# Optimization experiments

Measured on AMD Instinct MI355X. Metric: run time of the kernel, lower is better.

Reference implementation:

```python
import jax, jax.numpy as jnp
import numpy as np

B, L, D, H, M = 4, 2048, 256, 8, 256
HEAD = D // H
EPS = 1e-6


def _pos_embedding(maxlen, d):
    i = np.arange(maxlen, dtype=np.float64)[:, None]
    j = np.arange(d, dtype=np.float64)[None, :]
    angle = i / np.power(10000.0, (j - (j % 2)) / d)
    pe = np.where(j % 2 == 0, np.sin(angle), np.cos(angle))
    return jnp.asarray(pe, jnp.float32)  # [L, D]


def _projection_matrix(m, d, seed=0):
    # FAVOR+ orthogonal random features: one full QR block (m == d here),
    # rows rescaled by norms of iid Gaussian rows (scaling=0 in source).
    rng = np.random.default_rng(seed)
    block = rng.standard_normal((d, d))
    q, _ = np.linalg.qr(block)
    q = q.T[:m]
    mult = np.linalg.norm(rng.standard_normal((m, d)), axis=1)
    return jnp.asarray(mult[:, None] * q, jnp.float32)  # [M, D]


def _softmax_kernel(x, is_query, proj):
    # x: [B, L, H, D], proj: [M, D]
    d = x.shape[-1]
    m = proj.shape[0]
    x = x * (float(d) ** -0.25)
    xp = jnp.einsum('blhd,md->blhm', x, proj)
    diag = 0.5 * jnp.sum(x * x, axis=-1, keepdims=True)
    if is_query:
        mx = jnp.max(xp, axis=-1, keepdims=True)
    else:
        mx = jnp.max(xp, axis=(-3, -1), keepdims=True)  # over L and M
    return (float(m) ** -0.5) * (jnp.exp(xp - diag - mx) + EPS)


def setup_inputs() -> dict:
    key = jax.random.key(0)
    ks = jax.random.split(key, 12)
    s = 1.0 / np.sqrt(D)
    inp = {
        'query': jax.random.normal(ks[0], (B, L, D), jnp.float32),
        'key': jax.random.normal(ks[1], (B, L, D), jnp.float32),
        'value': jax.random.normal(ks[2], (B, L, D), jnp.float32),
        'mask': jnp.ones((B, L), jnp.float32),
        'Wq': jax.random.normal(ks[3], (D, D), jnp.float32) * s,
        'bq': jnp.zeros((D,), jnp.float32),
        'Wk': jax.random.normal(ks[4], (D, D), jnp.float32) * s,
        'bk': jnp.zeros((D,), jnp.float32),
        'Wv': jax.random.normal(ks[5], (D, D), jnp.float32) * s,
        'bv': jnp.zeros((D,), jnp.float32),
        'Wo': jax.random.normal(ks[6], (D, D), jnp.float32) * s,
        'bo': jnp.zeros((D,), jnp.float32),
        'proj': _projection_matrix(M, D, seed=0),
        'pos': _pos_embedding(L, D),
    }
    return inp


def reference(query, key, value, mask, Wq, bq, Wk, bk, Wv, bv, Wo, bo, proj, pos):
    b = query.shape[0]
    q = query @ Wq + bq                      # [B, L, D]
    k = key @ Wk + bk
    v = value @ Wv + bv
    # per-head copies keep the FULL model_size feature dim (as in source)
    q = jnp.broadcast_to(q[:, :, None, :], (b, L, H, D))
    k = jnp.broadcast_to(k[:, :, None, :], (b, L, H, D))
    pos_b = pos[None]                        # [1, L, D]
    cos_pos = jnp.repeat(pos_b[..., None, 1::2], 2, axis=-1)  # [1, L, 1, D]
    sin_pos = jnp.repeat(pos_b[..., None, ::2], 2, axis=-1)

    def rot(x):
        x2 = jnp.stack([-x[..., 1::2], x[..., ::2]], axis=-1).reshape(x.shape)
        return x * cos_pos + x2 * sin_pos

    q = rot(q)
    k = rot(k)
    v = v.reshape(b, L, H, HEAD)

    qp = _softmax_kernel(q, True, proj)      # [B, L, H, M]
    kp = _softmax_kernel(k, False, proj)     # [B, L, H, M]

    kvs = jnp.einsum('blhm,blhd->bhmd', kp, v)
    num = jnp.einsum('blhm,bhmd->blhd', qp, kvs)
    den = jnp.einsum('blhm,bhm->blh', qp, jnp.sum(kp, axis=1))
    ctx = (num / den[..., None]).reshape(b, L, D)
    return ctx @ Wo + bo
```

## Files before the change

### kernel.cpp

```cpp
#include <hip/hip_runtime.h>

typedef unsigned short u16;
typedef unsigned int u32;
typedef __bf16 bf16x8 __attribute__((ext_vector_type(8)));
typedef float f32x4 __attribute__((ext_vector_type(4)));

__device__ __forceinline__ float bf2f(u16 u) { return __uint_as_float(((u32)u) << 16); }
__device__ __forceinline__ u16 f2bf(float f) {
  u32 x = __float_as_uint(f);
  x += 0x7fffu + ((x >> 16) & 1u);
  return (u16)(x >> 16);
}
__device__ __forceinline__ u32 encf(float x) {
  u32 u = __float_as_uint(x);
  return (u >> 31) ? ~u : (u | 0x80000000u);
}
__device__ __forceinline__ float decf(u32 e) {
  return (e >> 31) ? __uint_as_float(e & 0x7fffffffu) : __uint_as_float(~e);
}

#define MFMA(a, b, c) __builtin_amdgcn_mfma_f32_16x16x32_bf16(a, b, c, 0, 0, 0)

__global__ __launch_bounds__(256) void prep_w(
    const float* Wq, const float* Wk, const float* Wv, const float* Wo,
    const float* proj, const float* bv,
    u16* WqT, u16* WkT, u16* projb, u16* WWT, float* bw,
    float* __restrict__ ksum, u32* __restrict__ mxk) {
  __shared__ u16 tsh[32][33];
  __shared__ u16 As[64][40];
  __shared__ u16 Bs[64][40];
  const int z = blockIdx.z;
  const int x = threadIdx.x, y = threadIdx.y;
  const int tid = y * 32 + x;
  if (z < 2) {
    const float* s = z == 0 ? Wq : Wk;
    u16* d = z == 0 ? WqT : WkT;
    int r0 = blockIdx.y * 32, c0 = blockIdx.x * 32;
#pragma unroll
    for (int i = 0; i < 32; i += 8) tsh[y + i][x] = f2bf(s[(r0 + y + i) * 256 + c0 + x]);
    __syncthreads();
#pragma unroll
    for (int i = 0; i < 32; i += 8) d[(c0 + y + i) * 256 + r0 + x] = tsh[x][y + i];
    return;
  }
  if (z == 2) {
    int r0 = blockIdx.y * 32, c0 = blockIdx.x * 32;
#pragma unroll
    for (int i = 0; i < 32; i += 8)
      projb[(r0 + y + i) * 256 + c0 + x] = f2bf(proj[(r0 + y + i) * 256 + c0 + x]);
    return;
  }
  if (blockIdx.x < 4 && blockIdx.y < 4) {
    const int o0 = blockIdx.x * 64, i0 = blockIdx.y * 64;
    const int lane = tid & 63, wid = tid >> 6;
    const int wm = (wid >> 1) * 32, wn = (wid & 1) * 32;
    const int fm = lane & 15, fq = (lane >> 4) * 8, rowq = (lane >> 4) * 4;
    const int dr = tid >> 3, oc = (tid & 7) * 8;
    const int ir = tid >> 2, dc = (tid & 3) * 8;
    f32x4 acc[2][2] = {};
    for (int it = 0; it < 8; ++it) {
      int d0 = it * 32;
      float4 w0 = *(const float4*)(Wo + (d0 + dr) * 256 + o0 + oc);
      float4 w1 = *(const float4*)(Wo + (d0 + dr) * 256 + o0 + oc + 4);
      float4 v0 = *(const float4*)(Wv + (i0 + ir) * 256 + d0 + dc);
      float4 v1 = *(const float4*)(Wv + (i0 + ir) * 256 + d0 + dc + 4);
      __syncthreads();
      float wv[8] = {w0.x, w0.y, w0.z, w0.w, w1.x, w1.y, w1.z, w1.w};
#pragma unroll
      for (int j = 0; j < 8; ++j) As[oc + j][dr] = f2bf(wv[j]);
      u16* bp = &Bs[ir][dc];
      bp[0] = f2bf(v0.x); bp[1] = f2bf(v0.y); bp[2] = f2bf(v0.z); bp[3] = f2bf(v0.w);
      bp[4] = f2bf(v1.x); bp[5] = f2bf(v1.y); bp[6] = f2bf(v1.z); bp[7] = f2bf(v1.w);
      __syncthreads();
      bf16x8 a0 = *(const bf16x8*)&As[wm + fm][fq];
      bf16x8 a1 = *(const bf16x8*)&As[wm + 16 + fm][fq];
      bf16x8 b0 = *(const bf16x8*)&Bs[wn + fm][fq];
      bf16x8 b1 = *(const bf16x8*)&Bs[wn + 16 + fm][fq];
      acc[0][0] = MFMA(a0, b0, acc[0][0]);
      acc[0][1] = MFMA(a0, b1, acc[0][1]);
      acc[1][0] = MFMA(a1, b0, acc[1][0]);
      acc[1][1] = MFMA(a1, b1, acc[1][1]);
    }
#pragma unroll
    for (int mt = 0; mt < 2; ++mt)
#pragma unroll
      for (int nt = 0; nt < 2; ++nt)
#pragma unroll
        for (int r = 0; r < 4; ++r)
          WWT[(o0 + wm + mt * 16 + rowq + r) * 256 + i0 + wn + nt * 16 + fm] =
              f2bf(acc[mt][nt][r]);
    return;
  }
  if (blockIdx.x == 4 && blockIdx.y == 0) {
    float s = 0.0f;
    for (int d = 0; d < 256; ++d) s = fmaf(bv[d], Wo[d * 256 + tid], s);
    bw[tid] = s;
    for (int i = tid; i < 1024; i += 256) ksum[i] = 0.0f;
    if (tid < 4) mxk[tid] = 0u;
  }
}

__global__ __launch_bounds__(256, 3) void projrot2(
    const float* __restrict__ Xq, const float* __restrict__ Xk,
    const u16* __restrict__ WqT, const u16* __restrict__ WkT,
    const float* __restrict__ bq, const float* __restrict__ bk,
    const float* __restrict__ pos, const u16* __restrict__ projb,
    float* __restrict__ diag_k, u16* __restrict__ qp,
    float* __restrict__ xp, u32* __restrict__ mxk) {
  const int mode = blockIdx.z;
  const float* X = mode ? Xq : Xk;
  const u16* W = mode ? WqT : WkT;
  const float* bias = mode ? bq : bk;
  __shared__ u16 As[32][40];
  __shared__ u16 Bs[256][40];
  __shared__ u16 cbuf[32][264];
  __shared__ float dred[2][32];
  __shared__ float mred[2][32];
  __shared__ float wred[4];
  const int row0 = blockIdx.x * 32;
  const int t = threadIdx.x;
  const int lane = t & 63, wid = t >> 6;
  const int wrow = wid & 1, wcol = wid >> 1;
  const int fm = lane & 15, fq = (lane >> 4) * 8, rowq = (lane >> 4) * 4;
  const int ar = t >> 3, ak = (t & 7) * 4;

  f32x4 acc[8] = {};
  float4 av = *(const float4*)(X + (long long)(row0 + ar) * 256 + ak);
  uint4 bv0 = ((const uint4*)(W + (long long)t * 256))[0];
  uint4 bv1 = ((const uint4*)(W + (long long)t * 256))[1];
  uint4 bv2 = ((const uint4*)(W + (long long)t * 256))[2];
  uint4 bv3 = ((const uint4*)(W + (long long)t * 256))[3];
  for (int s = 0; s < 8; ++s) {
    __syncthreads();
    As[ar][ak] = f2bf(av.x); As[ar][ak + 1] = f2bf(av.y);
    As[ar][ak + 2] = f2bf(av.z); As[ar][ak + 3] = f2bf(av.w);
    uint4* bsp = (uint4*)&Bs[t][0];
    bsp[0] = bv0; bsp[1] = bv1; bsp[2] = bv2; bsp[3] = bv3;
    __syncthreads();
    if (s < 7) {
      const int k1 = (s + 1) * 32;
      av = *(const float4*)(X + (long long)(row0 + ar) * 256 + k1 + ak);
      const uint4* wn = (const uint4*)(W + (long long)t * 256 + k1);
      bv0 = wn[0]; bv1 = wn[1]; bv2 = wn[2]; bv3 = wn[3];
    }
    bf16x8 af = *(const bf16x8*)&As[wrow * 16 + fm][fq];
#pragma unroll
    for (int j = 0; j < 8; ++j) {
      bf16x8 bf = *(const bf16x8*)&Bs[wcol * 128 + j * 16 + fm][fq];
      acc[j] = MFMA(af, bf, acc[j]);
    }
  }

  float dsum[4] = {};
#pragma unroll
  for (int j = 0; j < 8; ++j) {
    float bb2 = bias[wcol * 128 + j * 16 + fm];
#pragma unroll
    for (int r = 0; r < 4; ++r) {
      float v = acc[j][r] + bb2;
      acc[j][r] = v;
      dsum[r] += v * v;
    }
  }
#pragma unroll
  for (int o = 1; o < 16; o <<= 1)
#pragma unroll
    for (int r = 0; r < 4; ++r) dsum[r] += __shfl_xor(dsum[r], o, 64);
  if (fm == 0) {
#pragma unroll
    for (int r = 0; r < 4; ++r) dred[wcol][wrow * 16 + rowq + r] = dsum[r];
  }
  __syncthreads();
  if (mode == 0 && t < 32) diag_k[row0 + t] = 0.03125f * (dred[0][t] + dred[1][t]);

#pragma unroll
  for (int j = 0; j < 8; ++j) {
    const int c = wcol * 128 + j * 16 + fm;
#pragma unroll
    for (int r = 0; r < 4; ++r) {
      const int row = wrow * 16 + rowq + r;
      const int l = (row0 + row) & 2047;
      float v = acc[j][r];
      float prt = __shfl_xor(v, 1, 64);
      float x2 = (fm & 1) ? prt : -prt;
      float2 cs = *(const float2*)(pos + (long long)l * 256 + (c & ~1));
      cbuf[row][c] = f2bf(0.25f * (v * cs.y + x2 * cs.x));
    }
  }

  f32x4 acc2[8] = {};
  uint4 pv0 = ((const uint4*)(projb + (long long)t * 256))[0];
  uint4 pv1 = ((const uint4*)(projb + (long long)t * 256))[1];
  uint4 pv2 = ((const uint4*)(projb + (long long)t * 256))[2];
  uint4 pv3 = ((const uint4*)(projb + (long long)t * 256))[3];
  for (int s = 0; s < 8; ++s) {
    __syncthreads();
    uint4* bsp = (uint4*)&Bs[t][0];
    bsp[0] = pv0; bsp[1] = pv1; bsp[2] = pv2; bsp[3] = pv3;
    __syncthreads();
    if (s < 7) {
      const uint4* pn = (const uint4*)(projb + (long long)t * 256 + (s + 1) * 32);
      pv0 = pn[0]; pv1 = pn[1]; pv2 = pn[2]; pv3 = pn[3];
    }
    bf16x8 af = *(const bf16x8*)&cbuf[wrow * 16 + fm][s * 32 + fq];
#pragma unroll
    for (int j = 0; j < 8; ++j) {
      bf16x8 bf = *(const bf16x8*)&Bs[wcol * 128 + j * 16 + fm][fq];
      acc2[j] = MFMA(af, bf, acc2[j]);
    }
  }

  if (mode == 1) {
    float m4[4] = {-3.0e38f, -3.0e38f, -3.0e38f, -3.0e38f};
#pragma unroll
    for (int j = 0; j < 8; ++j)
#pragma unroll
      for (int r = 0; r < 4; ++r) m4[r] = fmaxf(m4[r], acc2[j][r]);
#pragma unroll
    for (int o = 1; o < 16; o <<= 1)
#pragma unroll
      for (int r = 0; r < 4; ++r) m4[r] = fmaxf(m4[r], __shfl_xor(m4[r], o, 64));
    if (fm == 0) {
#pragma unroll
      for (int r = 0; r < 4; ++r) mred[wcol][wrow * 16 + rowq + r] = m4[r];
    }
    __syncthreads();
#pragma unroll
    for (int j = 0; j < 8; ++j) {
      const int col = wcol * 128 + j * 16 + fm;
#pragma unroll
      for (int r = 0; r < 4; ++r) {
        const int row = wrow * 16 + rowq + r;
        float mxr = fmaxf(mred[0][row], mred[1][row]);
        float dgr = 0.03125f * (dred[0][row] + dred[1][row]);
        float v = 0.0625f * (__expf(acc2[j][r] - dgr - mxr) + 1e-6f);
        qp[(long long)(row0 + row) * 256 + col] = f2bf(v);
      }
    }
  } else {
    float mx = -3.0e38f;
#pragma unroll
    for (int j = 0; j < 8; ++j) {
      int col = wcol * 128 + j * 16 + fm;
#pragma unroll
      for (int r = 0; r < 4; ++r) {
        float v = acc2[j][r];
        xp[(long long)(row0 + wrow * 16 + rowq + r) * 256 + col] = v;
        mx = fmaxf(mx, v);
      }
    }
#pragma unroll
    for (int o = 32; o > 0; o >>= 1) mx = fmaxf(mx, __shfl_xor(mx, o, 64));
    if (lane == 0) wred[wid] = mx;
    __syncthreads();
    if (t == 0) {
      float m = fmaxf(fmaxf(wred[0], wred[1]), fmaxf(wred[2], wred[3]));
      atomicMax(mxk + (row0 >> 11), encf(m));
    }
  }
}

__global__ __launch_bounds__(256, 2) void kvs_raw_split(
    const float* __restrict__ xp, const float* __restrict__ Xv,
    const float* __restrict__ diag_k, const u32* __restrict__ mxk,
    float* __restrict__ part, float* __restrict__ ksum) {
  __shared__ union USM {
    struct { u16 As[64][40]; u16 Bs[64][40]; } s;
    float ksbuf[32][65];
  } sm;
  const int mxt = blockIdx.x, ny = blockIdx.y, z = blockIdx.z;
  const int b = z >> 3, kc = z & 7;
  const long long l0 = (long long)b * 2048 + kc * 256;
  const int t = threadIdx.x;
  const int lane = t & 63, wid = t >> 6;
  const int wrow = wid >> 1, wcol = wid & 1;
  const int fm = lane & 15, fq = (lane >> 4) * 8, rowq = (lane >> 4) * 4;
  const float mxv = decf(mxk[b]);
  const int sr = t >> 3, sc = (t & 7) * 8;
  f32x4 acc[2][2] = {};
  float ksp[8] = {};
  long long lrow = l0 + sr;
  float4 x0 = *(const float4*)(xp + lrow * 256 + mxt * 64 + sc);
  float4 x1 = *(const float4*)(xp + lrow * 256 + mxt * 64 + sc + 4);
  float4 v0 = *(const float4*)(Xv + lrow * 256 + ny * 64 + sc);
  float4 v1 = *(const float4*)(Xv + lrow * 256 + ny * 64 + sc + 4);
  float dgl = diag_k[lrow];
  for (int s = 0; s < 8; ++s) {
    float xv[8] = {x0.x, x0.y, x0.z, x0.w, x1.x, x1.y, x1.z, x1.w};
    float vv[8] = {v0.x, v0.y, v0.z, v0.w, v1.x, v1.y, v1.z, v1.w};
    u16 kpv[8], vpv[8];
#pragma unroll
    for (int j = 0; j < 8; ++j) {
      float v = 0.0625f * (__expf(xv[j] - dgl - mxv) + 1e-6f);
      kpv[j] = f2bf(v);
      ksp[j] += bf2f(kpv[j]);
      vpv[j] = f2bf(vv[j]);
    }
    __syncthreads();
#pragma unroll
    for (int j = 0; j < 8; ++j) {
      sm.s.As[sc + j][sr] = kpv[j];
      sm.s.Bs[sc + j][sr] = vpv[j];
    }
    __syncthreads();
    if (s < 7) {
      lrow = l0 + (s + 1) * 32 + sr;
      x0 = *(const float4*)(xp + lrow * 256 + mxt * 64 + sc);
      x1 = *(const float4*)(xp + lrow * 256 + mxt * 64 + sc + 4);
      v0 = *(const float4*)(Xv + lrow * 256 + ny * 64 + sc);
      v1 = *(const float4*)(Xv + lrow * 256 + ny * 64 + sc + 4);
      dgl = diag_k[lrow];
    }
    bf16x8 a0 = *(const bf16x8*)&sm.s.As[wrow * 32 + fm][fq];
    bf16x8 a1 = *(const bf16x8*)&sm.s.As[wrow * 32 + 16 + fm][fq];
    bf16x8 b0 = *(const bf16x8*)&sm.s.Bs[wcol * 32 + fm][fq];
    bf16x8 b1 = *(const bf16x8*)&sm.s.Bs[wcol * 32 + 16 + fm][fq];
    acc[0][0] = MFMA(a0, b0, acc[0][0]);
    acc[0][1] = MFMA(a0, b1, acc[0][1]);
    acc[1][0] = MFMA(a1, b0, acc[1][0]);
    acc[1][1] = MFMA(a1, b1, acc[1][1]);
  }
#pragma unroll
  for (int mt = 0; mt < 2; ++mt)
#pragma unroll
    for (int nt = 0; nt < 2; ++nt)
#pragma unroll
      for (int r = 0; r < 4; ++r)
        part[(long long)z * 65536 +
             (long long)(mxt * 64 + wrow * 32 + mt * 16 + rowq + r) * 256 +
             ny * 64 + wcol * 32 + nt * 16 + fm] = acc[mt][nt][r];
  __syncthreads();
#pragma unroll
  for (int j = 0; j < 8; ++j) sm.ksbuf[sr][sc + j] = ksp[j];
  __syncthreads();
  if (ny == 0 && t < 64) {
    float ssum = 0.0f;
    for (int r = 0; r < 32; ++r) ssum += sm.ksbuf[r][t];
    atomicAdd(ksum + b * 256 + mxt * 64 + t, ssum);
  }
}

__global__ __launch_bounds__(256) void kvsw(
    const u16* __restrict__ WWT, const float* __restrict__ part,
    const float* __restrict__ ksum, const float* __restrict__ bw,
    u16* __restrict__ kvsWT) {
  __shared__ u16 As[64][40];
  __shared__ u16 Bs[64][40];
  const int o0 = blockIdx.x * 64, m0 = blockIdx.y * 64, b = blockIdx.z;
  const int t = threadIdx.x;
  const int lane = t & 63, wid = t >> 6;
  const int wm = (wid >> 1) * 32, wn = (wid & 1) * 32;
  const int fm = lane & 15, fq = (lane >> 4) * 8, rowq = (lane >> 4) * 4;
  const int arow = t >> 2, acol = (t & 3) * 8;
  f32x4 acc[2][2] = {};
  for (int it = 0; it < 8; ++it) {
    int k0 = it * 32;
    uint4 av = *(const uint4*)(WWT + (o0 + arow) * 256 + k0 + acol);
    float4 s0 = {0, 0, 0, 0}, s1 = {0, 0, 0, 0};
#pragma unroll
    for (int kc = 0; kc < 8; ++kc) {
      const float* pp = part + (long long)(b * 8 + kc) * 65536 + (long long)(m0 + arow) * 256 + k0 + acol;
      float4 u0 = *(const float4*)(pp);
      float4 u1 = *(const float4*)(pp + 4);
      s0.x += u0.x; s0.y += u0.y; s0.z += u0.z; s0.w += u0.w;
      s1.x += u1.x; s1.y += u1.y; s1.z += u1.z; s1.w += u1.w;
    }
    __syncthreads();
    *(uint4*)&As[arow][acol] = av;
    u16* bp = &Bs[arow][acol];
    bp[0] = f2bf(s0.x); bp[1] = f2bf(s0.y); bp[2] = f2bf(s0.z); bp[3] = f2bf(s0.w);
    bp[4] = f2bf(s1.x); bp[5] = f2bf(s1.y); bp[6] = f2bf(s1.z); bp[7] = f2bf(s1.w);
    __syncthreads();
    bf16x8 a0 = *(const bf16x8*)&As[wm + fm][fq];
    bf16x8 a1 = *(const bf16x8*)&As[wm + 16 + fm][fq];
    bf16x8 b0 = *(const bf16x8*)&Bs[wn + fm][fq];
    bf16x8 b1 = *(const bf16x8*)&Bs[wn + 16 + fm][fq];
    acc[0][0] = MFMA(a0, b0, acc[0][0]);
    acc[0][1] = MFMA(a0, b1, acc[0][1]);
    acc[1][0] = MFMA(a1, b0, acc[1][0]);
    acc[1][1] = MFMA(a1, b1, acc[1][1]);
  }
#pragma unroll
  for (int mt = 0; mt < 2; ++mt)
#pragma unroll
    for (int nt = 0; nt < 2; ++nt) {
      int col = m0 + wn + nt * 16 + fm;
      float ksv = ksum[b * 256 + col];
#pragma unroll
      for (int r = 0; r < 4; ++r) {
        int row = o0 + wm + mt * 16 + rowq + r;
        float v = acc[mt][nt][r] + bw[row] * ksv;
        kvsWT[(long long)b * 65536 + (long long)row * 256 + col] = f2bf(v);
      }
    }
}

__global__ __launch_bounds__(256, 4) void numout(
    const u16* __restrict__ qp, const float* __restrict__ ksum,
    const u16* __restrict__ kvsWT, const float* __restrict__ bo,
    float* __restrict__ out) {
  __shared__ float ksm[256], dsh[16];
  const int row0 = blockIdx.x * 16;
  const int b = blockIdx.z;
  const long long qrow = (long long)b * 2048 + row0;
  const int t = threadIdx.x;
  const int lane = t & 63, wid = t >> 6;
  const int fm = lane & 15, fq = (lane >> 4) * 8, rowq = (lane >> 4) * 4;

  const u16* qa = qp + (qrow + fm) * 256 + fq;
  bf16x8 af[8];
#pragma unroll
  for (int it = 0; it < 8; ++it) af[it] = *(const bf16x8*)(qa + it * 32);

  const u16* kvb = kvsWT + (long long)b * 65536 + (long long)(wid * 64 + fm) * 256 + fq;
  bf16x8 bb[2][4];
#pragma unroll
  for (int j = 0; j < 4; ++j) bb[0][j] = *(const bf16x8*)(kvb + j * 4096);

  ksm[t] = ksum[b * 256 + t];
  const int prow = t >> 4, pc0 = (t & 15) * 16;
  const u16* qr = qp + (qrow + prow) * 256 + pc0;
  uint4 u0 = *(const uint4*)(qr);
  uint4 u1 = *(const uint4*)(qr + 8);
  __syncthreads();

  float denp = 0.0f;
  u32 uu[8] = {u0.x, u0.y, u0.z, u0.w, u1.x, u1.y, u1.z, u1.w};
#pragma unroll
  for (int j = 0; j < 8; ++j) {
    denp += bf2f((u16)(uu[j] & 0xffffu)) * ksm[pc0 + 2 * j];
    denp += bf2f((u16)(uu[j] >> 16)) * ksm[pc0 + 2 * j + 1];
  }
#pragma unroll
  for (int o = 1; o < 16; o <<= 1) denp += __shfl_xor(denp, o, 64);
  if ((t & 15) == 0) dsh[prow] = denp;

  f32x4 acc[4] = {};
#pragma unroll
  for (int it = 0; it < 8; ++it) {
    if (it < 7) {
#pragma unroll
      for (int j = 0; j < 4; ++j)
        bb[(it + 1) & 1][j] = *(const bf16x8*)(kvb + j * 4096 + (it + 1) * 32);
    }
#pragma unroll
    for (int j = 0; j < 4; ++j) acc[j] = MFMA(af[it], bb[it & 1][j], acc[j]);
  }
  __syncthreads();
#pragma unroll
  for (int j = 0; j < 4; ++j) {
    int col = wid * 64 + j * 16 + fm;
    float bb2 = bo[col];
#pragma unroll
    for (int r = 0; r < 4; ++r) {
      int l = rowq + r;
      out[(qrow + l) * 256 + col] = acc[j][r] / dsh[l] + bb2;
    }
  }
}

extern "C" void kernel_launch(void* const* d_in, const int* in_sizes, int n_in,
                              void* d_out, int out_size, void* d_ws, size_t ws_size,
                              hipStream_t stream) {
  (void)in_sizes; (void)n_in; (void)out_size; (void)ws_size;
  const float* query = (const float*)d_in[0];
  const float* key = (const float*)d_in[1];
  const float* value = (const float*)d_in[2];
  const float* Wq = (const float*)d_in[4];
  const float* bq = (const float*)d_in[5];
  const float* Wk = (const float*)d_in[6];
  const float* bk = (const float*)d_in[7];
  const float* Wv = (const float*)d_in[8];
  const float* bv = (const float*)d_in[9];
  const float* Wo = (const float*)d_in[10];
  const float* bo = (const float*)d_in[11];
  const float* proj = (const float*)d_in[12];
  const float* pos = (const float*)d_in[13];

  char* w = (char*)d_ws;
  u16* qp = (u16*)(w);
  float* xp = (float*)(w + (8 << 20));
  float* part = (float*)(w + (16 << 20));
  u16* kvsWT = (u16*)(w + (24 << 20));
  u16* WqT = (u16*)(w + (25 << 20));
  u16* WkT = WqT + 65536;
  u16* projb = WkT + 65536;
  u16* WWT = projb + 65536;
  float* diag_k = (float*)(w + (26 << 20));
  float* ksum = diag_k + 8192;
  float* bw = ksum + 1024;
  u32* mxk = (u32*)(bw + 256);

  prep_w<<<dim3(8, 8, 4), dim3(32, 8), 0, stream>>>(Wq, Wk, Wv, Wo, proj, bv,
                                                    WqT, WkT, projb, WWT, bw,
                                                    ksum, mxk);
  projrot2<<<dim3(256, 1, 2), dim3(256), 0, stream>>>(
      query, key, WqT, WkT, bq, bk, pos, projb, diag_k, qp, xp, mxk);
  kvs_raw_split<<<dim3(4, 4, 32), dim3(256), 0, stream>>>(xp, value, diag_k, mxk,
                                                          part, ksum);
  kvsw<<<dim3(4, 4, 4), dim3(256), 0, stream>>>(WWT, part, ksum, bw, kvsWT);
  numout<<<dim3(128, 1, 4), dim3(256), 0, stream>>>(qp, ksum, kvsWT, bo,
                                                    (float*)d_out);
}
```

Measured before the change: 81.77 us.

## Halve KV split count and stage numout operands through shared memory

The key/value reduction now splits L into 4 chunks of 512 instead of 8 of 256. This halves the partial buffers and the summation work in kvsw, though each block runs a longer serial loop and there are fewer blocks overall. numout no longer loads MFMA fragments directly from global memory. It stages the q tile and the kvs matrix through LDS with coalesced row loads and double-buffered register prefetch, which adds two barriers per k-step. Workspace offsets are compacted to match the smaller partial buffer.

```diff
diff --git a/kernel.cpp b/kernel.cpp
--- a/kernel.cpp
+++ b/kernel.cpp
@@ -260,7 +260,7 @@
   }
 }
 
-__global__ __launch_bounds__(256, 2) void kvs_raw_split(
+__global__ __launch_bounds__(256) void kvs_raw_split(
     const float* __restrict__ xp, const float* __restrict__ Xv,
     const float* __restrict__ diag_k, const u32* __restrict__ mxk,
     float* __restrict__ part, float* __restrict__ ksum) {
@@ -269,8 +269,8 @@
     float ksbuf[32][65];
   } sm;
   const int mxt = blockIdx.x, ny = blockIdx.y, z = blockIdx.z;
-  const int b = z >> 3, kc = z & 7;
-  const long long l0 = (long long)b * 2048 + kc * 256;
+  const int b = z >> 2, kc = z & 3;
+  const long long l0 = (long long)b * 2048 + kc * 512;
   const int t = threadIdx.x;
   const int lane = t & 63, wid = t >> 6;
   const int wrow = wid >> 1, wcol = wid & 1;
@@ -285,7 +285,7 @@
   float4 v0 = *(const float4*)(Xv + lrow * 256 + ny * 64 + sc);
   float4 v1 = *(const float4*)(Xv + lrow * 256 + ny * 64 + sc + 4);
   float dgl = diag_k[lrow];
-  for (int s = 0; s < 8; ++s) {
+  for (int s = 0; s < 16; ++s) {
     float xv[8] = {x0.x, x0.y, x0.z, x0.w, x1.x, x1.y, x1.z, x1.w};
     float vv[8] = {v0.x, v0.y, v0.z, v0.w, v1.x, v1.y, v1.z, v1.w};
     u16 kpv[8], vpv[8];
@@ -303,7 +303,7 @@
       sm.s.Bs[sc + j][sr] = vpv[j];
     }
     __syncthreads();
-    if (s < 7) {
+    if (s < 15) {
       lrow = l0 + (s + 1) * 32 + sr;
       x0 = *(const float4*)(xp + lrow * 256 + mxt * 64 + sc);
       x1 = *(const float4*)(xp + lrow * 256 + mxt * 64 + sc + 4);
@@ -358,8 +358,8 @@
     uint4 av = *(const uint4*)(WWT + (o0 + arow) * 256 + k0 + acol);
     float4 s0 = {0, 0, 0, 0}, s1 = {0, 0, 0, 0};
 #pragma unroll
-    for (int kc = 0; kc < 8; ++kc) {
-      const float* pp = part + (long long)(b * 8 + kc) * 65536 + (long long)(m0 + arow) * 256 + k0 + acol;
+    for (int kc = 0; kc < 4; ++kc) {
+      const float* pp = part + (long long)(b * 4 + kc) * 65536 + (long long)(m0 + arow) * 256 + k0 + acol;
       float4 u0 = *(const float4*)(pp);
       float4 u1 = *(const float4*)(pp + 4);
       s0.x += u0.x; s0.y += u0.y; s0.z += u0.z; s0.w += u0.w;
@@ -399,6 +399,8 @@
     const u16* __restrict__ qp, const float* __restrict__ ksum,
     const u16* __restrict__ kvsWT, const float* __restrict__ bo,
     float* __restrict__ out) {
+  __shared__ u16 As[16][40];
+  __shared__ u16 Bs[256][40];
   __shared__ float ksm[256], dsh[16];
   const int row0 = blockIdx.x * 16;
   const int b = blockIdx.z;
@@ -406,16 +408,14 @@
   const int t = threadIdx.x;
   const int lane = t & 63, wid = t >> 6;
   const int fm = lane & 15, fq = (lane >> 4) * 8, rowq = (lane >> 4) * 4;
-
-  const u16* qa = qp + (qrow + fm) * 256 + fq;
-  bf16x8 af[8];
-#pragma unroll
-  for (int it = 0; it < 8; ++it) af[it] = *(const bf16x8*)(qa + it * 32);
-
-  const u16* kvb = kvsWT + (long long)b * 65536 + (long long)(wid * 64 + fm) * 256 + fq;
-  bf16x8 bb[2][4];
-#pragma unroll
-  for (int j = 0; j < 4; ++j) bb[0][j] = *(const bf16x8*)(kvb + j * 4096);
+  const int ar = t >> 4, ak = (t & 15) * 2;
+
+  u32 a0 = *(const u32*)(qp + (qrow + ar) * 256 + ak);
+  const u16* kvr = kvsWT + (long long)b * 65536 + (long long)t * 256;
+  uint4 bv0 = ((const uint4*)kvr)[0];
+  uint4 bv1 = ((const uint4*)kvr)[1];
+  uint4 bv2 = ((const uint4*)kvr)[2];
+  uint4 bv3 = ((const uint4*)kvr)[3];
 
   ksm[t] = ksum[b * 256 + t];
   const int prow = t >> 4, pc0 = (t & 15) * 16;
@@ -436,17 +436,25 @@
   if ((t & 15) == 0) dsh[prow] = denp;
 
   f32x4 acc[4] = {};
-#pragma unroll
-  for (int it = 0; it < 8; ++it) {
-    if (it < 7) {
-#pragma unroll
-      for (int j = 0; j < 4; ++j)
-        bb[(it + 1) & 1][j] = *(const bf16x8*)(kvb + j * 4096 + (it + 1) * 32);
-    }
-#pragma unroll
-    for (int j = 0; j < 4; ++j) acc[j] = MFMA(af[it], bb[it & 1][j], acc[j]);
-  }
-  __syncthreads();
+  for (int s = 0; s < 8; ++s) {
+    __syncthreads();
+    *(u32*)&As[ar][ak] = a0;
+    uint4* bsp = (uint4*)&Bs[t][0];
+    bsp[0] = bv0; bsp[1] = bv1; bsp[2] = bv2; bsp[3] = bv3;
+    __syncthreads();
+    if (s < 7) {
+      const int k1 = (s + 1) * 32;
+      a0 = *(const u32*)(qp + (qrow + ar) * 256 + k1 + ak);
+      const uint4* kn = (const uint4*)(kvr + k1);
+      bv0 = kn[0]; bv1 = kn[1]; bv2 = kn[2]; bv3 = kn[3];
+    }
+    bf16x8 af = *(const bf16x8*)&As[fm][fq];
+#pragma unroll
+    for (int j = 0; j < 4; ++j) {
+      bf16x8 bf = *(const bf16x8*)&Bs[wid * 64 + j * 16 + fm][fq];
+      acc[j] = MFMA(af, bf, acc[j]);
+    }
+  }
 #pragma unroll
   for (int j = 0; j < 4; ++j) {
     int col = wid * 64 + j * 16 + fm;
@@ -481,12 +489,12 @@
   u16* qp = (u16*)(w);
   float* xp = (float*)(w + (8 << 20));
   float* part = (float*)(w + (16 << 20));
-  u16* kvsWT = (u16*)(w + (24 << 20));
-  u16* WqT = (u16*)(w + (25 << 20));
+  u16* kvsWT = (u16*)(w + (20 << 20));
+  u16* WqT = (u16*)(w + (21 << 20));
   u16* WkT = WqT + 65536;
   u16* projb = WkT + 65536;
   u16* WWT = projb + 65536;
-  float* diag_k = (float*)(w + (26 << 20));
+  float* diag_k = (float*)(w + (22 << 20));
   float* ksum = diag_k + 8192;
   float* bw = ksum + 1024;
   u32* mxk = (u32*)(bw + 256);
@@ -496,7 +504,7 @@
                                                     ksum, mxk);
   projrot2<<<dim3(256, 1, 2), dim3(256), 0, stream>>>(
       query, key, WqT, WkT, bq, bk, pos, projb, diag_k, qp, xp, mxk);
-  kvs_raw_split<<<dim3(4, 4, 32), dim3(256), 0, stream>>>(xp, value, diag_k, mxk,
+  kvs_raw_split<<<dim3(4, 4, 16), dim3(256), 0, stream>>>(xp, value, diag_k, mxk,
                                                           part, ksum);
   kvsw<<<dim3(4, 4, 4), dim3(256), 0, stream>>>(WWT, part, ksum, bw, kvsWT);
   numout<<<dim3(128, 1, 4), dim3(256), 0, stream>>>(qp, ksum, kvsWT, bo,
```

After: 81.12 us. About the same (-0.8%).
